# Kernel optimization log

Measured on AMD Instinct MI355X. Metric: run time of the kernel, lower is better.

## Reference

```python
import jax, jax.numpy as jnp
import numpy as np

N, E, V, H, HEADS, L, B = 20000, 320000, 100, 128, 3, 2, 200
NEG = 0.2   # leaky_relu negative_slope
EPS = 1e-5  # LayerNorm eps


def _mean_nodes(x, gid):
    # dgl.mean_nodes: per-graph mean of node features
    s = jax.ops.segment_sum(x, gid, num_segments=B)
    c = jax.ops.segment_sum(jnp.ones((x.shape[0], 1), x.dtype), gid, num_segments=B)
    return s / jnp.maximum(c, 1.0)


def _gat_layer(h, src, dst, Wn, bn, att, Ws, b, gamma, beta):
    # weight_node: Linear(H, H*HEADS)
    wv = (h @ Wn + bn).reshape(-1, HEADS, H)
    u = wv[src]  # [E, heads, H] gathered src features
    # attn = leaky_relu(sum(cat(u, v) * w_att)) split into u/v halves (no concat materialized)
    attn = (jnp.einsum('ehd,hd->eh', u, att[:, :H])
            + jnp.einsum('ehd,hd->eh', wv[dst], att[:, H:]))
    attn = jax.nn.leaky_relu(attn, NEG)  # [E, heads]
    # segment softmax over incoming edges of each dst node (mailbox softmax)
    m = jax.ops.segment_max(attn, dst, num_segments=N)
    m = jnp.where(jnp.isfinite(m), m, 0.0)
    e = jnp.exp(attn - m[dst])
    s = jax.ops.segment_sum(e, dst, num_segments=N)
    score = e / s[dst]
    agg = jax.ops.segment_sum(score[:, :, None] * u, dst, num_segments=N)  # [N, heads, H]
    res = agg.reshape(-1, HEADS * H) @ Ws + b
    # DGL leaves zero-in-degree nodes with zero reduced features (reduce_func never runs)
    has_in = jax.ops.segment_sum(jnp.ones((E,), h.dtype), dst, num_segments=N) > 0
    res = jnp.where(has_in[:, None], res, 0.0)
    x = res + h  # residual, then LayerNorm, relu (dropout is eval-mode identity)
    mu = jnp.mean(x, -1, keepdims=True)
    var = jnp.var(x, -1, keepdims=True)
    x = (x - mu) * jax.lax.rsqrt(var + EPS) * gamma + beta
    return jax.nn.relu(x)


def _gru_dir(x, Wih, Whh, bih, bhh, reverse):
    # torch nn.GRU single direction; x: [B, T, in]
    def step(hprev, xt):
        gi = xt @ Wih.T + bih
        gh = hprev @ Whh.T + bhh
        ir, iz, inn = jnp.split(gi, 3, -1)
        hr, hz, hn = jnp.split(gh, 3, -1)
        r = jax.nn.sigmoid(ir + hr)
        z = jax.nn.sigmoid(iz + hz)
        n = jnp.tanh(inn + r * hn)
        hnew = (1.0 - z) * n + z * hprev
        return hnew, hnew
    h0 = jnp.zeros((x.shape[0], Whh.shape[1]), x.dtype)
    hT, ys = jax.lax.scan(step, h0, jnp.swapaxes(x, 0, 1), reverse=reverse)
    return jnp.swapaxes(ys, 0, 1), hT


def setup_inputs() -> dict:
    key = jax.random.key(0)
    k = jax.random.split(key, 16)
    sc = 0.05
    return {
        'h': jax.random.normal(k[0], (N, H), jnp.float32),
        'wid': jax.random.randint(k[1], (N,), 0, V),
        'src': jax.random.randint(k[2], (E,), 0, N),
        'dst': jax.random.randint(k[3], (E,), 0, N),
        'graph_ids': jnp.sort(jax.random.randint(k[4], (N,), 0, B)),
        'proj_W': jax.random.normal(k[5], (V + H, H), jnp.float32) * sc,
        'proj_b': jnp.zeros((H,), jnp.float32),
        'conv_Wn': jax.random.normal(k[6], (L, H, HEADS * H), jnp.float32) * sc,
        'conv_bn': jnp.zeros((L, HEADS * H), jnp.float32),
        'conv_att': jax.random.normal(k[7], (L, HEADS, 2 * H), jnp.float32) * sc,
        'conv_Ws': jax.random.normal(k[8], (L, HEADS * H, H), jnp.float32) * sc,
        'conv_b': jnp.zeros((L, H), jnp.float32),
        'conv_gamma': jnp.ones((L, H), jnp.float32),
        'conv_beta': jnp.zeros((L, H), jnp.float32),
        'gru_Wih0': jax.random.normal(k[9], (2, 3 * H, H), jnp.float32) * sc,
        'gru_Whh0': jax.random.normal(k[10], (2, 3 * H, H), jnp.float32) * sc,
        'gru_bih0': jnp.zeros((2, 3 * H), jnp.float32),
        'gru_bhh0': jnp.zeros((2, 3 * H), jnp.float32),
        'gru_Wih1': jax.random.normal(k[11], (2, 3 * H, 2 * H), jnp.float32) * sc,
        'gru_Whh1': jax.random.normal(k[12], (2, 3 * H, H), jnp.float32) * sc,
        'gru_bih1': jnp.zeros((2, 3 * H), jnp.float32),
        'gru_bhh1': jnp.zeros((2, 3 * H), jnp.float32),
    }


def reference(h, wid, src, dst, graph_ids, proj_W, proj_b, conv_Wn, conv_bn, conv_att, conv_Ws, conv_b, conv_gamma, conv_beta, gru_Wih0, gru_Whh0, gru_bih0, gru_bhh0, gru_Wih1, gru_Whh1, gru_bih1, gru_bhh1):
    one_hot = jax.nn.one_hot(wid, V, dtype=h.dtype)
    hcur = jnp.concatenate([one_hot, h], -1) @ proj_W + proj_b  # project
    readouts = [_mean_nodes(hcur, graph_ids)]
    for l in range(L):
        hcur = _gat_layer(hcur, src, dst, conv_Wn[l], conv_bn[l], conv_att[l],
                          conv_Ws[l], conv_b[l], conv_gamma[l], conv_beta[l])
        readouts.append(_mean_nodes(hcur, graph_ids))
    x = jnp.stack(readouts, 1)  # [B, L+1, H] GRU readout sequence
    finals = []
    for (Wih, Whh, bih, bhh) in ((gru_Wih0, gru_Whh0, gru_bih0, gru_bhh0),
                                 (gru_Wih1, gru_Whh1, gru_bih1, gru_bhh1)):
        yf, hf = _gru_dir(x, Wih[0], Whh[0], bih[0], bhh[0], False)
        yb, hb = _gru_dir(x, Wih[1], Whh[1], bih[1], bhh[1], True)
        x = jnp.concatenate([yf, yb], -1)
        finals += [hf, hb]
    # torch returns h_n [num_layers*2, B, H]; module takes mean over dim 0
    return jnp.mean(jnp.stack(finals, 0), 0)  # [B, H]
```

## Files before the change

### kernel.cpp

```cpp
#include <hip/hip_runtime.h>
#include <cstddef>
#include <cstdint>

static constexpr int Nn    = 20000;
static constexpr int Ee    = 320000;
static constexpr int Vv    = 100;
static constexpr int Hh    = 128;
static constexpr int HEADS = 3;
static constexpr int Bb    = 200;
static constexpr float NEG = 0.2f;
static constexpr float EPS = 1e-5f;

typedef short bf16x8 __attribute__((ext_vector_type(8)));
typedef float f32x4  __attribute__((ext_vector_type(4)));

__device__ inline unsigned short bf16_rne(float x) {
    unsigned u = __builtin_bit_cast(unsigned, x);
    u += 0x7FFFu + ((u >> 16) & 1u);
    return (unsigned short)(u >> 16);
}
__device__ inline float bf16_f(unsigned short h) {
    unsigned u = ((unsigned)h) << 16;
    return __builtin_bit_cast(float, u);
}
__device__ inline float bf_lo(unsigned u) { return __builtin_bit_cast(float, u << 16); }
__device__ inline float bf_hi(unsigned u) { return __builtin_bit_cast(float, u & 0xFFFF0000u); }
__device__ inline float lrelu(float a) { return a >= 0.f ? a : NEG * a; }
__device__ inline float sigmoidf(float x) { return 1.f / (1.f + __expf(-x)); }

__global__ __launch_bounds__(1024) void scan_offsets(const int* __restrict__ deg,
                                                     int* __restrict__ offs,
                                                     int* __restrict__ cur) {
    __shared__ int sums[1024];
    const int tid = threadIdx.x;
    const int per = (Nn + 1023) >> 10;
    int begin = tid * per;
    int end = begin + per; if (end > Nn) end = Nn;
    if (begin > Nn) begin = Nn;
    int s = 0;
    for (int i = begin; i < end; i++) s += deg[i];
    sums[tid] = s;
    __syncthreads();
    for (int off = 1; off < 1024; off <<= 1) {
        int v = (tid >= off) ? sums[tid - off] : 0;
        __syncthreads();
        sums[tid] += v;
        __syncthreads();
    }
    int run = sums[tid] - s;
    for (int i = begin; i < end; i++) {
        offs[i] = run; cur[i] = run;
        run += deg[i];
    }
    if (end == Nn) offs[Nn] = run;
}

__global__ void fill_csr(const int* __restrict__ dst, const int* __restrict__ src,
                         int* __restrict__ cur, int* __restrict__ csrc) {
    for (int i = blockIdx.x * blockDim.x + threadIdx.x; i < Ee; i += gridDim.x * blockDim.x) {
        int p = atomicAdd(&cur[dst[i]], 1);
        csrc[p] = src[i];
    }
}

struct PrepArgs {
    const float *projW, *convWn, *convWs, *convAtt, *convBn, *convB;
    const float *Wih0, *Whh0, *Wih1, *Whh1;
    const int *gid, *dst;
    unsigned short *pBth, *pBtl;
    unsigned short *WfTh0, *WfTl0, *WfTh1, *WfTl1;
    float *vavd, *vc, *biasF;
    float *WihT0, *WhhT0, *WihT1, *WhhT1;
    int *goffs, *deg;
};

__device__ inline void wsplit(const float* B, int K, int N, int idx,
                              unsigned short* Bth, unsigned short* Btl) {
    int k = idx / N, n = idx - k * N;
    float v = B[idx];
    unsigned short h = bf16_rne(v);
    unsigned short l = bf16_rne(v - bf16_f(h));
    Bth[(size_t)n * K + k] = h;
    Btl[(size_t)n * K + k] = l;
}
__device__ inline void gruT(const float* W, int K, int idx, float* WT) {
    int d = idx / (384 * K);
    int r = idx - d * 384 * K;
    int j = r / K, k = r - j * K;
    WT[(size_t)d * K * 384 + (size_t)k * 384 + j] = W[idx];
}

__global__ void prep_all(PrepArgs a) {
    int i = blockIdx.x * blockDim.x + threadIdx.x;
    if (i < 16384) { wsplit(a.projW, 128, 128, i, a.pBth, a.pBtl); return; } i -= 16384;
#pragma unroll
    for (int l = 0; l < 2; l++) {
        if (i < 49152) {
            int k = i >> 7, c = i & 127;
            int h = k >> 7, i_ = k & 127;
            const float* wn = a.convWn + (size_t)l * 49152 + (size_t)i_ * 384 + h * 128;
            const float* ws = a.convWs + (size_t)l * 49152 + (size_t)(h * 128) * 128 + c;
            float v = 0.f;
            for (int j = 0; j < 128; j++) v += wn[j] * ws[(size_t)j * 128];
            unsigned short hi = bf16_rne(v);
            unsigned short lo = bf16_rne(v - bf16_f(hi));
            unsigned short* th = l ? a.WfTh1 : a.WfTh0;
            unsigned short* tl = l ? a.WfTl1 : a.WfTl0;
            th[(size_t)c * 384 + k] = hi;
            tl[(size_t)c * 384 + k] = lo;
            return;
        }
        i -= 49152;
    }
    if (i < 1536) {
        int l = i / 768, r = i % 768;
        int sd = r / 384, rr = r % 384, h = rr >> 7, i_ = rr & 127;
        const float* wn = a.convWn + (size_t)l * 49152 + (size_t)i_ * 384 + h * 128;
        const float* at = a.convAtt + l * 768 + h * 256 + sd * 128;
        float v = 0.f;
        for (int j = 0; j < 128; j++) v += wn[j] * at[j];
        a.vavd[i] = v;
        return;
    } i -= 1536;
    if (i < 12) {
        int l = i / 6, r = i % 6, sd = r / 3, h = r % 3;
        const float* bn = a.convBn + l * 384 + h * 128;
        const float* at = a.convAtt + l * 768 + h * 256 + sd * 128;
        float v = 0.f;
        for (int j = 0; j < 128; j++) v += bn[j] * at[j];
        a.vc[i] = v;
        return;
    } i -= 12;
    if (i < 256) {
        int l = i >> 7, c = i & 127;
        const float* bn = a.convBn + l * 384;
        const float* ws = a.convWs + (size_t)l * 49152 + c;
        float v = a.convB[l * 128 + c];
        for (int k = 0; k < 384; k++) v += bn[k] * ws[(size_t)k * 128];
        a.biasF[i] = v;
        return;
    } i -= 256;
    if (i < 98304)  { gruT(a.Wih0, 128, i, a.WihT0); return; }  i -= 98304;
    if (i < 98304)  { gruT(a.Whh0, 128, i, a.WhhT0); return; }  i -= 98304;
    if (i < 196608) { gruT(a.Wih1, 256, i, a.WihT1); return; }  i -= 196608;
    if (i < 98304)  { gruT(a.Whh1, 128, i, a.WhhT1); return; }  i -= 98304;
    if (i < Nn) {
        int g = a.gid[i];
        if (i == 0) { for (int b = 0; b <= g; b++) a.goffs[b] = 0; }
        else { int pg = a.gid[i - 1]; for (int b = pg + 1; b <= g; b++) a.goffs[b] = i; }
        if (i == Nn - 1) { for (int b = g + 1; b <= Bb; b++) a.goffs[b] = Nn; }
        return;
    } i -= Nn;
    if (i < Ee) atomicAdd(&a.deg[a.dst[i]], 1);
}

struct GArgs {
    const float* A; const unsigned short* Bth; const unsigned short* Btl;
    const float* bias; int M, K;
    const int* wid; const float* projW;
    const int* deg; const float* gamma; const float* beta;
    float* hcur;
    const int* gid; float* reado;
    const float* vavd; const float* vc;
    float* adf; float* addf;
    unsigned short* hb;
};

template <int MODE>
__global__ __launch_bounds__(256) void gemm_fused(GArgs a) {
    __shared__ unsigned short As_hi[32][40];
    __shared__ unsigned short As_lo[32][40];
    __shared__ unsigned short Bs_hi[128][40];
    __shared__ unsigned short Bs_lo[128][40];
    __shared__ float ytile[32][132];
    __shared__ float sred[6][32][4];
    __shared__ int sgid[32];
    const int tid  = threadIdx.x;
    const int row0 = blockIdx.y * 32;
    const int wn   = tid >> 6;
    const int L    = tid & 63;
    const int lrow = L & 15;
    const int lq   = L >> 4;
    const int K = a.K;

    f32x4 acc[2][2];
#pragma unroll
    for (int i = 0; i < 2; i++)
#pragma unroll
        for (int j = 0; j < 2; j++) acc[i][j] = (f32x4){0.f, 0.f, 0.f, 0.f};

    for (int kb = 0; kb < K; kb += 32) {
        {
            int m  = tid >> 3;
            int kq = (tid & 7) * 4;
            float4 v = *(const float4*)(a.A + (size_t)(row0 + m) * K + kb + kq);
            unsigned short h0 = bf16_rne(v.x), h1 = bf16_rne(v.y),
                           h2 = bf16_rne(v.z), h3 = bf16_rne(v.w);
            *(short4*)&As_hi[m][kq] = make_short4((short)h0, (short)h1, (short)h2, (short)h3);
            *(short4*)&As_lo[m][kq] = make_short4((short)bf16_rne(v.x - bf16_f(h0)),
                                                  (short)bf16_rne(v.y - bf16_f(h1)),
                                                  (short)bf16_rne(v.z - bf16_f(h2)),
                                                  (short)bf16_rne(v.w - bf16_f(h3)));
        }
        {
            int n  = tid >> 1;
            int kh = (tid & 1) * 16;
            const unsigned short* sh = a.Bth + (size_t)n * K + kb + kh;
            const unsigned short* sl = a.Btl + (size_t)n * K + kb + kh;
            *(float4*)&Bs_hi[n][kh]     = *(const float4*)sh;
            *(float4*)&Bs_hi[n][kh + 8] = *(const float4*)(sh + 8);
            *(float4*)&Bs_lo[n][kh]     = *(const float4*)sl;
            *(float4*)&Bs_lo[n][kh + 8] = *(const float4*)(sl + 8);
        }
        __syncthreads();
        bf16x8 ah[2], al[2], bh[2], bl[2];
#pragma unroll
        for (int mi = 0; mi < 2; mi++) {
            int r = mi * 16 + lrow;
            ah[mi] = *(const bf16x8*)&As_hi[r][lq * 8];
            al[mi] = *(const bf16x8*)&As_lo[r][lq * 8];
        }
#pragma unroll
        for (int ni = 0; ni < 2; ni++) {
            int r = wn * 32 + ni * 16 + lrow;
            bh[ni] = *(const bf16x8*)&Bs_hi[r][lq * 8];
            bl[ni] = *(const bf16x8*)&Bs_lo[r][lq * 8];
        }
#pragma unroll
        for (int mi = 0; mi < 2; mi++)
#pragma unroll
            for (int ni = 0; ni < 2; ni++) {
                acc[mi][ni] = __builtin_amdgcn_mfma_f32_16x16x32_bf16(ah[mi], bh[ni], acc[mi][ni], 0, 0, 0);
                acc[mi][ni] = __builtin_amdgcn_mfma_f32_16x16x32_bf16(ah[mi], bl[ni], acc[mi][ni], 0, 0, 0);
                acc[mi][ni] = __builtin_amdgcn_mfma_f32_16x16x32_bf16(al[mi], bh[ni], acc[mi][ni], 0, 0, 0);
            }
        __syncthreads();
    }

#pragma unroll
    for (int ni = 0; ni < 2; ni++) {
        float bb = a.bias[wn * 32 + ni * 16 + lrow];
#pragma unroll
        for (int mi = 0; mi < 2; mi++)
#pragma unroll
            for (int r = 0; r < 4; r++) acc[mi][ni][r] += bb;
    }

    if constexpr (MODE == 0) {
#pragma unroll
        for (int mi = 0; mi < 2; mi++)
#pragma unroll
            for (int r = 0; r < 4; r++) {
                int lr = mi * 16 + lq * 4 + r;
                int row = row0 + lr;
                int wi = a.wid[row];
#pragma unroll
                for (int ni = 0; ni < 2; ni++) {
                    int c = wn * 32 + ni * 16 + lrow;
                    float y = acc[mi][ni][r] + a.projW[(size_t)wi * 128 + c];
                    acc[mi][ni][r] = y;
                    a.hcur[(size_t)row * 128 + c] = y;
                    ytile[lr][c] = y;
                }
            }
    }

    if constexpr (MODE == 2) {
        __shared__ float red1[32][4], red2[32][4];
        float g4[2], be4[2];
#pragma unroll
        for (int ni = 0; ni < 2; ni++) {
            int c = wn * 32 + ni * 16 + lrow;
            g4[ni] = a.gamma[c]; be4[ni] = a.beta[c];
        }
#pragma unroll
        for (int mi = 0; mi < 2; mi++)
#pragma unroll
            for (int r = 0; r < 4; r++) {
                int lr = mi * 16 + lq * 4 + r;
                int row = row0 + lr;
                int dg = a.deg[row];
#pragma unroll
                for (int ni = 0; ni < 2; ni++) {
                    int c = wn * 32 + ni * 16 + lrow;
                    float hold = a.hcur[(size_t)row * 128 + c];
                    acc[mi][ni][r] = hold + (dg > 0 ? acc[mi][ni][r] : 0.f);
                }
            }
#pragma unroll
        for (int mi = 0; mi < 2; mi++)
#pragma unroll
            for (int r = 0; r < 4; r++) {
                float ps = acc[mi][0][r] + acc[mi][1][r];
#pragma unroll
                for (int o = 1; o < 16; o <<= 1) ps += __shfl_xor(ps, o, 64);
                if (lrow == 0) red1[mi * 16 + lq * 4 + r][wn] = ps;
            }
        __syncthreads();
#pragma unroll
        for (int mi = 0; mi < 2; mi++)
#pragma unroll
            for (int r = 0; r < 4; r++) {
                int lr = mi * 16 + lq * 4 + r;
                float mu = (red1[lr][0] + red1[lr][1] + red1[lr][2] + red1[lr][3]) * (1.f / 128.f);
                float qs = 0.f;
#pragma unroll
                for (int ni = 0; ni < 2; ni++) {
                    float dx = acc[mi][ni][r] - mu;
                    qs += dx * dx;
                }
#pragma unroll
                for (int o = 1; o < 16; o <<= 1) qs += __shfl_xor(qs, o, 64);
                if (lrow == 0) red2[lr][wn] = qs;
            }
        __syncthreads();
#pragma unroll
        for (int mi = 0; mi < 2; mi++)
#pragma unroll
            for (int r = 0; r < 4; r++) {
                int lr = mi * 16 + lq * 4 + r;
                int row = row0 + lr;
                float mu = (red1[lr][0] + red1[lr][1] + red1[lr][2] + red1[lr][3]) * (1.f / 128.f);
                float var = (red2[lr][0] + red2[lr][1] + red2[lr][2] + red2[lr][3]) * (1.f / 128.f);
                float rs = rsqrtf(var + EPS);
#pragma unroll
                for (int ni = 0; ni < 2; ni++) {
                    int c = wn * 32 + ni * 16 + lrow;
                    float y = fmaxf((acc[mi][ni][r] - mu) * rs * g4[ni] + be4[ni], 0.f);
                    acc[mi][ni][r] = y;
                    a.hcur[(size_t)row * 128 + c] = y;
                    ytile[lr][c] = y;
                }
            }
    }

    if (tid < 32) sgid[tid] = a.gid[row0 + tid];

    const bool dots = (a.vavd != nullptr);
    if (dots) {
        float vv0[6], vv1[6];
#pragma unroll
        for (int d = 0; d < 6; d++) {
            vv0[d] = a.vavd[d * 128 + wn * 32 + lrow];
            vv1[d] = a.vavd[d * 128 + wn * 32 + 16 + lrow];
        }
#pragma unroll
        for (int d = 0; d < 6; d++) {
#pragma unroll
            for (int mi = 0; mi < 2; mi++)
#pragma unroll
                for (int r = 0; r < 4; r++) {
                    float ps = acc[mi][0][r] * vv0[d] + acc[mi][1][r] * vv1[d];
#pragma unroll
                    for (int o = 1; o < 16; o <<= 1) ps += __shfl_xor(ps, o, 64);
                    if (lrow == 0) sred[d][mi * 16 + lq * 4 + r][wn] = ps;
                }
        }
    }
    __syncthreads();

    {
        int j = tid & 127, hh = tid >> 7;
        float sum = 0.f; int curg = -1;
        for (int r = hh * 16; r < hh * 16 + 16; r++) {
            int g = sgid[r];
            if (g != curg) {
                if (curg >= 0) atomicAdd(&a.reado[(size_t)curg * 128 + j], sum);
                sum = 0.f; curg = g;
            }
            sum += ytile[r][j];
        }
        if (curg >= 0) atomicAdd(&a.reado[(size_t)curg * 128 + j], sum);
    }

    if (dots) {
        if (tid < 192) {
            int row = tid & 31, d = tid >> 5;
            float s = sred[d][row][0] + sred[d][row][1] + sred[d][row][2] + sred[d][row][3]
                    + a.vc[d];
            int node = row0 + row;
            int sd = d / 3, h = d - sd * 3;
            float* dstp = sd ? a.addf : a.adf;
            dstp[(size_t)node * 4 + h] = s;
        }
        {
            int row = tid >> 3, c0 = (tid & 7) * 16;
            unsigned* dst = (unsigned*)(a.hb + (size_t)(row0 + row) * 128 + c0);
#pragma unroll
            for (int q = 0; q < 8; q++) {
                unsigned lo = bf16_rne(ytile[row][c0 + 2 * q]);
                unsigned hi = bf16_rne(ytile[row][c0 + 2 * q + 1]);
                dst[q] = lo | (hi << 16);
            }
        }
    }
}

__global__ __launch_bounds__(256) void gat_gather(const unsigned short* __restrict__ hb,
                                                  const float4* __restrict__ ad,
                                                  const float4* __restrict__ add,
                                                  const int* __restrict__ offs,
                                                  const int* __restrict__ csrc,
                                                  float* __restrict__ T) {
    __shared__ float4 slot[4][64];
    const int n = (blockIdx.x * 256 + threadIdx.x) >> 6;
    const int wv_ = threadIdx.x >> 6;
    const int L = threadIdx.x & 63;
    if (n >= Nn) return;
    const int start = offs[n];
    const int deg = offs[n + 1] - start;
    float2* o2 = (float2*)(T + (size_t)n * 384);
    if (deg == 0) {
        float2 z = make_float2(0.f, 0.f);
        o2[L] = z; o2[64 + L] = z; o2[128 + L] = z;
        return;
    }
    const float4 adn = add[n];
    float2 t0 = make_float2(0.f, 0.f), t1 = t0, t2 = t0;

    if (deg <= 64) {
        int sn = 0; float e0 = 0.f, e1 = 0.f, e2 = 0.f;
        if (L < deg) {
            sn = csrc[start + L];
            float4 a4 = ad[sn];
            e0 = __expf(lrelu(a4.x + adn.x));
            e1 = __expf(lrelu(a4.y + adn.y));
            e2 = __expf(lrelu(a4.z + adn.z));
        }
        float s0 = e0, s1 = e1, s2 = e2;
#pragma unroll
        for (int o = 32; o > 0; o >>= 1) {
            s0 += __shfl_xor(s0, o, 64);
            s1 += __shfl_xor(s1, o, 64);
            s2 += __shfl_xor(s2, o, 64);
        }
        slot[wv_][L] = make_float4(__builtin_bit_cast(float, sn),
                                   e0 / s0, e1 / s1, e2 / s2);
        __builtin_amdgcn_wave_barrier();
#pragma unroll 2
        for (int j = 0; j < deg; j++) {
            float4 sc = slot[wv_][j];
            int s_n = __builtin_bit_cast(int, sc.x);
            unsigned u = ((const unsigned*)(hb + (size_t)s_n * 128))[L];
            float x0 = bf_lo(u), x1 = bf_hi(u);
            t0.x += sc.y * x0; t0.y += sc.y * x1;
            t1.x += sc.z * x0; t1.y += sc.z * x1;
            t2.x += sc.w * x0; t2.y += sc.w * x1;
        }
    } else {
        float s0 = 0.f, s1 = 0.f, s2 = 0.f;
        for (int i = L; i < deg; i += 64) {
            int sn = csrc[start + i];
            float4 a4 = ad[sn];
            s0 += __expf(lrelu(a4.x + adn.x));
            s1 += __expf(lrelu(a4.y + adn.y));
            s2 += __expf(lrelu(a4.z + adn.z));
        }
#pragma unroll
        for (int o = 32; o > 0; o >>= 1) {
            s0 += __shfl_xor(s0, o, 64);
            s1 += __shfl_xor(s1, o, 64);
            s2 += __shfl_xor(s2, o, 64);
        }
        float i0 = 1.f / s0, i1 = 1.f / s1, i2 = 1.f / s2;
        for (int base = 0; base < deg; base += 64) {
            int cnt = deg - base; if (cnt > 64) cnt = 64;
            if (L < cnt) {
                int sn = csrc[start + base + L];
                float4 a4 = ad[sn];
                slot[wv_][L] = make_float4(__builtin_bit_cast(float, sn),
                                           __expf(lrelu(a4.x + adn.x)) * i0,
                                           __expf(lrelu(a4.y + adn.y)) * i1,
                                           __expf(lrelu(a4.z + adn.z)) * i2);
            }
            __builtin_amdgcn_wave_barrier();
            for (int j = 0; j < cnt; j++) {
                float4 sc = slot[wv_][j];
                int s_n = __builtin_bit_cast(int, sc.x);
                unsigned u = ((const unsigned*)(hb + (size_t)s_n * 128))[L];
                float x0 = bf_lo(u), x1 = bf_hi(u);
                t0.x += sc.y * x0; t0.y += sc.y * x1;
                t1.x += sc.z * x0; t1.y += sc.z * x1;
                t2.x += sc.w * x0; t2.y += sc.w * x1;
            }
            __builtin_amdgcn_wave_barrier();
        }
    }
    o2[L] = t0; o2[64 + L] = t1; o2[128 + L] = t2;
}

__global__ __launch_bounds__(768) void gru_all(const float* __restrict__ reado,
                                               const int* __restrict__ goffs,
                                               const float* __restrict__ WihT0,
                                               const float* __restrict__ WhhT0,
                                               const float* __restrict__ bih0,
                                               const float* __restrict__ bhh0,
                                               const float* __restrict__ WihT1,
                                               const float* __restrict__ WhhT1,
                                               const float* __restrict__ bih1,
                                               const float* __restrict__ bhh1,
                                               float* __restrict__ out) {
    const int b = blockIdx.x;
    const int tid = threadIdx.x;
    const int dir = tid / 384;
    const int j = tid - dir * 384;
    __shared__ float xs[3][128];
    __shared__ float y0s[3][256];
    __shared__ float hs[2][128];
    __shared__ float gil[2][384], ghl[2][384];
    __shared__ float fin01[2][128];
    if (tid < 128) {
        int cnt = goffs[b + 1] - goffs[b];
        float invc = 1.f / fmaxf((float)cnt, 1.f);
#pragma unroll
        for (int t = 0; t < 3; t++)
            xs[t][tid] = reado[(size_t)t * Bb * Hh + (size_t)b * Hh + tid] * invc;
    }
    if (j < 128) hs[dir][j] = 0.f;
    __syncthreads();
    {
        const float* Wi = WihT0 + (size_t)dir * 128 * 384;
        const float* Wh = WhhT0 + (size_t)dir * 128 * 384;
        float gi[3];
        gi[0] = gi[1] = gi[2] = bih0[dir * 384 + j];
        for (int k = 0; k < 128; k++) {
            float w = Wi[(size_t)k * 384 + j];
            gi[0] += w * xs[0][k]; gi[1] += w * xs[1][k]; gi[2] += w * xs[2][k];
        }
        const float bhj = bhh0[dir * 384 + j];
        for (int step = 0; step < 3; step++) {
            int t = dir ? 2 - step : step;
            float g = bhj;
            for (int k = 0; k < 128; k++) g += Wh[(size_t)k * 384 + j] * hs[dir][k];
            ghl[dir][j] = g;
            gil[dir][j] = gi[t];
            __syncthreads();
            if (j < 128) {
                float r = sigmoidf(gil[dir][j] + ghl[dir][j]);
                float z = sigmoidf(gil[dir][j + 128] + ghl[dir][j + 128]);
                float nn2 = tanhf(gil[dir][j + 256] + r * ghl[dir][j + 256]);
                float hnew = (1.f - z) * nn2 + z * hs[dir][j];
                hs[dir][j] = hnew;
                y0s[t][dir * 128 + j] = hnew;
                if (step == 2) fin01[dir][j] = hnew;
            }
            __syncthreads();
        }
    }
    if (j < 128) hs[dir][j] = 0.f;
    {
        const float* Wi = WihT1 + (size_t)dir * 256 * 384;
        const float* Wh = WhhT1 + (size_t)dir * 128 * 384;
        float gi[3];
        gi[0] = gi[1] = gi[2] = bih1[dir * 384 + j];
        for (int k = 0; k < 256; k++) {
            float w = Wi[(size_t)k * 384 + j];
            gi[0] += w * y0s[0][k]; gi[1] += w * y0s[1][k]; gi[2] += w * y0s[2][k];
        }
        const float bhj = bhh1[dir * 384 + j];
        __syncthreads();
        for (int step = 0; step < 3; step++) {
            int t = dir ? 2 - step : step;
            float g = bhj;
            for (int k = 0; k < 128; k++) g += Wh[(size_t)k * 384 + j] * hs[dir][k];
            ghl[dir][j] = g;
            gil[dir][j] = gi[t];
            __syncthreads();
            if (j < 128) {
                float r = sigmoidf(gil[dir][j] + ghl[dir][j]);
                float z = sigmoidf(gil[dir][j + 128] + ghl[dir][j + 128]);
                float nn2 = tanhf(gil[dir][j + 256] + r * ghl[dir][j + 256]);
                float hnew = (1.f - z) * nn2 + z * hs[dir][j];
                hs[dir][j] = hnew;
                if (step == 2) xs[dir][j] = hnew;
            }
            __syncthreads();
        }
    }
    if (tid < 128)
        out[(size_t)b * Hh + tid] = 0.25f * (fin01[0][tid] + fin01[1][tid] +
                                             xs[0][tid] + xs[1][tid]);
}

extern "C" void kernel_launch(void* const* d_in, const int* in_sizes, int n_in,
                              void* d_out, int out_size, void* d_ws, size_t ws_size,
                              hipStream_t stream) {
    const float* h      = (const float*)d_in[0];
    const int*   wid    = (const int*)d_in[1];
    const int*   src    = (const int*)d_in[2];
    const int*   dst    = (const int*)d_in[3];
    const int*   gid    = (const int*)d_in[4];
    const float* projW  = (const float*)d_in[5];
    const float* projB  = (const float*)d_in[6];
    const float* convWn = (const float*)d_in[7];
    const float* convBn = (const float*)d_in[8];
    const float* convAtt= (const float*)d_in[9];
    const float* convWs = (const float*)d_in[10];
    const float* convB  = (const float*)d_in[11];
    const float* convG  = (const float*)d_in[12];
    const float* convBe = (const float*)d_in[13];
    const float* Wih0   = (const float*)d_in[14];
    const float* Whh0   = (const float*)d_in[15];
    const float* bih0   = (const float*)d_in[16];
    const float* bhh0   = (const float*)d_in[17];
    const float* Wih1   = (const float*)d_in[18];
    const float* Whh1   = (const float*)d_in[19];
    const float* bih1   = (const float*)d_in[20];
    const float* bhh1   = (const float*)d_in[21];
    float* out = (float*)d_out;

    char* p = (char*)d_ws;
    auto align16 = [&]() { p = (char*)(((uintptr_t)p + 15) & ~(uintptr_t)15); };
    auto alloc_f = [&](size_t n) { align16(); float* r = (float*)p; p += n * sizeof(float); return r; };
    auto alloc_i = [&](size_t n) { align16(); int* r = (int*)p; p += n * sizeof(int); return r; };
    auto alloc_s = [&](size_t n) { align16(); unsigned short* r = (unsigned short*)p; p += n * sizeof(unsigned short); return r; };
    float* hcur  = alloc_f((size_t)Nn * 128);
    float* T     = alloc_f((size_t)Nn * 384);
    float* adbuf = alloc_f((size_t)Nn * 4);
    float* addbuf= alloc_f((size_t)Nn * 4);
    float* reado = alloc_f((size_t)3 * Bb * Hh);
    int* deg  = alloc_i(Nn);
    const size_t zero_bytes = (size_t)3 * Bb * Hh * sizeof(float) + Nn * sizeof(int);
    float* WihT0 = alloc_f((size_t)2 * 128 * 384);
    float* WhhT0 = alloc_f((size_t)2 * 128 * 384);
    float* WihT1 = alloc_f((size_t)2 * 256 * 384);
    float* WhhT1 = alloc_f((size_t)2 * 128 * 384);
    float* vavd  = alloc_f(1536);
    float* vc    = alloc_f(12);
    float* biasF = alloc_f(256);
    int* offs = alloc_i(Nn + 1);
    int* cur  = alloc_i(Nn);
    int* csrc = alloc_i(Ee);
    int* goffs = alloc_i(Bb + 1);
    unsigned short* hb = alloc_s((size_t)Nn * 128);
    unsigned short* pBth = alloc_s(128 * 128);
    unsigned short* pBtl = alloc_s(128 * 128);
    unsigned short* WfTh[2] = { alloc_s(128 * 384), alloc_s(128 * 384) };
    unsigned short* WfTl[2] = { alloc_s(128 * 384), alloc_s(128 * 384) };

    hipMemsetAsync(reado, 0, zero_bytes, stream);

    PrepArgs pa;
    pa.projW = projW + (size_t)Vv * Hh;
    pa.convWn = convWn; pa.convWs = convWs; pa.convAtt = convAtt;
    pa.convBn = convBn; pa.convB = convB;
    pa.Wih0 = Wih0; pa.Whh0 = Whh0; pa.Wih1 = Wih1; pa.Whh1 = Whh1;
    pa.gid = gid; pa.dst = dst;
    pa.pBth = pBth; pa.pBtl = pBtl;
    pa.WfTh0 = WfTh[0]; pa.WfTl0 = WfTl[0]; pa.WfTh1 = WfTh[1]; pa.WfTl1 = WfTl[1];
    pa.vavd = vavd; pa.vc = vc; pa.biasF = biasF;
    pa.WihT0 = WihT0; pa.WhhT0 = WhhT0; pa.WihT1 = WihT1; pa.WhhT1 = WhhT1;
    pa.goffs = goffs; pa.deg = deg;
    const int prep_total = 16384 + 2 * 49152 + 1536 + 12 + 256 + 98304 + 98304 + 196608 + 98304 + Nn + Ee;
    prep_all<<<(prep_total + 255) / 256, 256, 0, stream>>>(pa);

    scan_offsets<<<1, 1024, 0, stream>>>(deg, offs, cur);
    fill_csr<<<1250, 256, 0, stream>>>(dst, src, cur, csrc);

    {
        GArgs g = {};
        g.A = h; g.Bth = pBth; g.Btl = pBtl; g.bias = projB;
        g.M = Nn; g.K = 128;
        g.wid = wid; g.projW = projW; g.hcur = hcur;
        g.gid = gid; g.reado = reado;
        g.vavd = vavd; g.vc = vc; g.adf = adbuf; g.addf = addbuf; g.hb = hb;
        gemm_fused<0><<<dim3(1, Nn / 32), 256, 0, stream>>>(g);
    }

    const int nwaveblocks = (Nn * 64 + 255) / 256;
    for (int l = 0; l < 2; l++) {
        gat_gather<<<nwaveblocks, 256, 0, stream>>>(hb, (const float4*)adbuf, (const float4*)addbuf,
                                                    offs, csrc, T);
        {
            GArgs g = {};
            g.A = T; g.Bth = WfTh[l]; g.Btl = WfTl[l]; g.bias = biasF + l * 128;
            g.M = Nn; g.K = 384;
            g.deg = deg; g.gamma = convG + l * Hh; g.beta = convBe + l * Hh;
            g.hcur = hcur;
            g.gid = gid; g.reado = reado + (size_t)(l + 1) * Bb * Hh;
            if (l == 0) { g.vavd = vavd + 768; g.vc = vc + 6; g.adf = adbuf; g.addf = addbuf; g.hb = hb; }
            gemm_fused<2><<<dim3(1, Nn / 32), 256, 0, stream>>>(g);
        }
    }

    gru_all<<<Bb, 768, 0, stream>>>(reado, goffs, WihT0, WhhT0, bih0, bhh0,
                                    WihT1, WhhT1, bih1, bhh1, out);
}
```

Measured before the change: 371.8 us.

## Fuse GAT edge gather with output GEMM and LayerNorm into one per-layer kernel

Each GAT layer's gather/softmax-aggregation kernel and the following GEMM+LayerNorm kernel are merged into a single kernel. Aggregated features are split into bf16 hi/lo parts and kept in shared memory as the GEMM A operand, so the fp32 intermediate T buffer no longer has to be written to and read back from global memory. The tile shrinks to 16 rows per block, with 4 waves each gathering 4 nodes. The hb and attention-dot buffers are double-buffered so a layer never overwrites its own input. In exchange, blocks are smaller and each GEMM tile reloads the full weight matrix, which raises weight traffic and may reduce MFMA efficiency.

```diff
diff --git a/kernel.cpp b/kernel.cpp
--- a/kernel.cpp
+++ b/kernel.cpp
@@ -158,7 +158,6 @@
     const float* A; const unsigned short* Bth; const unsigned short* Btl;
     const float* bias; int M, K;
     const int* wid; const float* projW;
-    const int* deg; const float* gamma; const float* beta;
     float* hcur;
     const int* gid; float* reado;
     const float* vavd; const float* vc;
@@ -166,8 +165,7 @@
     unsigned short* hb;
 };
 
-template <int MODE>
-__global__ __launch_bounds__(256) void gemm_fused(GArgs a) {
+__global__ __launch_bounds__(256) void gemm_proj(GArgs a) {
     __shared__ unsigned short As_hi[32][40];
     __shared__ unsigned short As_lo[32][40];
     __shared__ unsigned short Bs_hi[128][40];
@@ -176,7 +174,7 @@
     __shared__ float sred[6][32][4];
     __shared__ int sgid[32];
     const int tid  = threadIdx.x;
-    const int row0 = blockIdx.y * 32;
+    const int row0 = blockIdx.x * 32;
     const int wn   = tid >> 6;
     const int L    = tid & 63;
     const int lrow = L & 15;
@@ -246,98 +244,26 @@
             for (int r = 0; r < 4; r++) acc[mi][ni][r] += bb;
     }
 
-    if constexpr (MODE == 0) {
-#pragma unroll
-        for (int mi = 0; mi < 2; mi++)
-#pragma unroll
-            for (int r = 0; r < 4; r++) {
-                int lr = mi * 16 + lq * 4 + r;
-                int row = row0 + lr;
-                int wi = a.wid[row];
-#pragma unroll
-                for (int ni = 0; ni < 2; ni++) {
-                    int c = wn * 32 + ni * 16 + lrow;
-                    float y = acc[mi][ni][r] + a.projW[(size_t)wi * 128 + c];
-                    acc[mi][ni][r] = y;
-                    a.hcur[(size_t)row * 128 + c] = y;
-                    ytile[lr][c] = y;
-                }
+#pragma unroll
+    for (int mi = 0; mi < 2; mi++)
+#pragma unroll
+        for (int r = 0; r < 4; r++) {
+            int lr = mi * 16 + lq * 4 + r;
+            int row = row0 + lr;
+            int wi = a.wid[row];
+#pragma unroll
+            for (int ni = 0; ni < 2; ni++) {
+                int c = wn * 32 + ni * 16 + lrow;
+                float y = acc[mi][ni][r] + a.projW[(size_t)wi * 128 + c];
+                acc[mi][ni][r] = y;
+                a.hcur[(size_t)row * 128 + c] = y;
+                ytile[lr][c] = y;
             }
-    }
-
-    if constexpr (MODE == 2) {
-        __shared__ float red1[32][4], red2[32][4];
-        float g4[2], be4[2];
-#pragma unroll
-        for (int ni = 0; ni < 2; ni++) {
-            int c = wn * 32 + ni * 16 + lrow;
-            g4[ni] = a.gamma[c]; be4[ni] = a.beta[c];
-        }
-#pragma unroll
-        for (int mi = 0; mi < 2; mi++)
-#pragma unroll
-            for (int r = 0; r < 4; r++) {
-                int lr = mi * 16 + lq * 4 + r;
-                int row = row0 + lr;
-                int dg = a.deg[row];
-#pragma unroll
-                for (int ni = 0; ni < 2; ni++) {
-                    int c = wn * 32 + ni * 16 + lrow;
-                    float hold = a.hcur[(size_t)row * 128 + c];
-                    acc[mi][ni][r] = hold + (dg > 0 ? acc[mi][ni][r] : 0.f);
-                }
-            }
-#pragma unroll
-        for (int mi = 0; mi < 2; mi++)
-#pragma unroll
-            for (int r = 0; r < 4; r++) {
-                float ps = acc[mi][0][r] + acc[mi][1][r];
-#pragma unroll
-                for (int o = 1; o < 16; o <<= 1) ps += __shfl_xor(ps, o, 64);
-                if (lrow == 0) red1[mi * 16 + lq * 4 + r][wn] = ps;
-            }
-        __syncthreads();
-#pragma unroll
-        for (int mi = 0; mi < 2; mi++)
-#pragma unroll
-            for (int r = 0; r < 4; r++) {
-                int lr = mi * 16 + lq * 4 + r;
-                float mu = (red1[lr][0] + red1[lr][1] + red1[lr][2] + red1[lr][3]) * (1.f / 128.f);
-                float qs = 0.f;
-#pragma unroll
-                for (int ni = 0; ni < 2; ni++) {
-                    float dx = acc[mi][ni][r] - mu;
-                    qs += dx * dx;
-                }
-#pragma unroll
-                for (int o = 1; o < 16; o <<= 1) qs += __shfl_xor(qs, o, 64);
-                if (lrow == 0) red2[lr][wn] = qs;
-            }
-        __syncthreads();
-#pragma unroll
-        for (int mi = 0; mi < 2; mi++)
-#pragma unroll
-            for (int r = 0; r < 4; r++) {
-                int lr = mi * 16 + lq * 4 + r;
-                int row = row0 + lr;
-                float mu = (red1[lr][0] + red1[lr][1] + red1[lr][2] + red1[lr][3]) * (1.f / 128.f);
-                float var = (red2[lr][0] + red2[lr][1] + red2[lr][2] + red2[lr][3]) * (1.f / 128.f);
-                float rs = rsqrtf(var + EPS);
-#pragma unroll
-                for (int ni = 0; ni < 2; ni++) {
-                    int c = wn * 32 + ni * 16 + lrow;
-                    float y = fmaxf((acc[mi][ni][r] - mu) * rs * g4[ni] + be4[ni], 0.f);
-                    acc[mi][ni][r] = y;
-                    a.hcur[(size_t)row * 128 + c] = y;
-                    ytile[lr][c] = y;
-                }
-            }
-    }
+        }
 
     if (tid < 32) sgid[tid] = a.gid[row0 + tid];
 
-    const bool dots = (a.vavd != nullptr);
-    if (dots) {
+    {
         float vv0[6], vv1[6];
 #pragma unroll
         for (int d = 0; d < 6; d++) {
@@ -373,9 +299,282 @@
         if (curg >= 0) atomicAdd(&a.reado[(size_t)curg * 128 + j], sum);
     }
 
+    if (tid < 192) {
+        int row = tid & 31, d = tid >> 5;
+        float s = sred[d][row][0] + sred[d][row][1] + sred[d][row][2] + sred[d][row][3]
+                + a.vc[d];
+        int node = row0 + row;
+        int sd = d / 3, h = d - sd * 3;
+        float* dstp = sd ? a.addf : a.adf;
+        dstp[(size_t)node * 4 + h] = s;
+    }
+    {
+        int row = tid >> 3, c0 = (tid & 7) * 16;
+        unsigned* dst = (unsigned*)(a.hb + (size_t)(row0 + row) * 128 + c0);
+#pragma unroll
+        for (int q = 0; q < 8; q++) {
+            unsigned lo = bf16_rne(ytile[row][c0 + 2 * q]);
+            unsigned hi = bf16_rne(ytile[row][c0 + 2 * q + 1]);
+            dst[q] = lo | (hi << 16);
+        }
+    }
+}
+
+struct LArgs {
+    const unsigned short* hbin;
+    const float4* ad; const float4* add;
+    const int* offs; const int* csrc;
+    const unsigned short* Bth; const unsigned short* Btl;
+    const float* biasF;
+    const float* gamma; const float* beta;
+    float* hcur;
+    const int* gid; float* reado;
+    const float* vavd; const float* vc;
+    float* adf; float* addf;
+    unsigned short* hbout;
+};
+
+__global__ __launch_bounds__(256) void gat_layer(LArgs a) {
+    __shared__ unsigned short Ah[16][392];
+    __shared__ unsigned short Al[16][392];
+    __shared__ unsigned short Bh[128][40];
+    __shared__ unsigned short Bl[128][40];
+    __shared__ float4 slot[4][64];
+    __shared__ float ytile[16][132];
+    __shared__ float sred[6][16][4];
+    __shared__ float red1[16][4], red2[16][4];
+    __shared__ int sgid[16];
+    __shared__ int sdeg[16];
+    const int tid  = threadIdx.x;
+    const int row0 = blockIdx.x * 16;
+    const int w    = tid >> 6;
+    const int L    = tid & 63;
+    const int lrow = L & 15;
+    const int lq   = L >> 4;
+
+    for (int nn = 0; nn < 4; nn++) {
+        const int lr = w * 4 + nn;
+        const int n = row0 + lr;
+        const int start = a.offs[n];
+        const int deg = a.offs[n + 1] - start;
+        if (L == 0) sdeg[lr] = deg;
+        float2 t0 = make_float2(0.f, 0.f), t1 = t0, t2 = t0;
+        if (deg > 0) {
+            const float4 adn = a.add[n];
+            if (deg <= 64) {
+                int sn = 0; float e0 = 0.f, e1 = 0.f, e2 = 0.f;
+                if (L < deg) {
+                    sn = a.csrc[start + L];
+                    float4 a4 = a.ad[sn];
+                    e0 = __expf(lrelu(a4.x + adn.x));
+                    e1 = __expf(lrelu(a4.y + adn.y));
+                    e2 = __expf(lrelu(a4.z + adn.z));
+                }
+                float s0 = e0, s1 = e1, s2 = e2;
+#pragma unroll
+                for (int o = 32; o > 0; o >>= 1) {
+                    s0 += __shfl_xor(s0, o, 64);
+                    s1 += __shfl_xor(s1, o, 64);
+                    s2 += __shfl_xor(s2, o, 64);
+                }
+                slot[w][L] = make_float4(__builtin_bit_cast(float, sn),
+                                         e0 / s0, e1 / s1, e2 / s2);
+                __builtin_amdgcn_wave_barrier();
+                for (int j = 0; j < deg; j++) {
+                    float4 sc = slot[w][j];
+                    int s_n = __builtin_bit_cast(int, sc.x);
+                    unsigned u = ((const unsigned*)a.hbin)[(size_t)s_n * 64 + L];
+                    float x0 = bf_lo(u), x1 = bf_hi(u);
+                    t0.x += sc.y * x0; t0.y += sc.y * x1;
+                    t1.x += sc.z * x0; t1.y += sc.z * x1;
+                    t2.x += sc.w * x0; t2.y += sc.w * x1;
+                }
+                __builtin_amdgcn_wave_barrier();
+            } else {
+                float s0 = 0.f, s1 = 0.f, s2 = 0.f;
+                for (int i = L; i < deg; i += 64) {
+                    int sn = a.csrc[start + i];
+                    float4 a4 = a.ad[sn];
+                    s0 += __expf(lrelu(a4.x + adn.x));
+                    s1 += __expf(lrelu(a4.y + adn.y));
+                    s2 += __expf(lrelu(a4.z + adn.z));
+                }
+#pragma unroll
+                for (int o = 32; o > 0; o >>= 1) {
+                    s0 += __shfl_xor(s0, o, 64);
+                    s1 += __shfl_xor(s1, o, 64);
+                    s2 += __shfl_xor(s2, o, 64);
+                }
+                float i0 = 1.f / s0, i1 = 1.f / s1, i2 = 1.f / s2;
+                for (int base = 0; base < deg; base += 64) {
+                    int cnt = deg - base; if (cnt > 64) cnt = 64;
+                    if (L < cnt) {
+                        int sn = a.csrc[start + base + L];
+                        float4 a4 = a.ad[sn];
+                        slot[w][L] = make_float4(__builtin_bit_cast(float, sn),
+                                                 __expf(lrelu(a4.x + adn.x)) * i0,
+                                                 __expf(lrelu(a4.y + adn.y)) * i1,
+                                                 __expf(lrelu(a4.z + adn.z)) * i2);
+                    }
+                    __builtin_amdgcn_wave_barrier();
+                    for (int j = 0; j < cnt; j++) {
+                        float4 sc = slot[w][j];
+                        int s_n = __builtin_bit_cast(int, sc.x);
+                        unsigned u = ((const unsigned*)a.hbin)[(size_t)s_n * 64 + L];
+                        float x0 = bf_lo(u), x1 = bf_hi(u);
+                        t0.x += sc.y * x0; t0.y += sc.y * x1;
+                        t1.x += sc.z * x0; t1.y += sc.z * x1;
+                        t2.x += sc.w * x0; t2.y += sc.w * x1;
+                    }
+                    __builtin_amdgcn_wave_barrier();
+                }
+            }
+        }
+        unsigned* ah32 = (unsigned*)&Ah[lr][0];
+        unsigned* al32 = (unsigned*)&Al[lr][0];
+        float2 tv[3] = {t0, t1, t2};
+#pragma unroll
+        for (int hd = 0; hd < 3; hd++) {
+            unsigned short hx = bf16_rne(tv[hd].x);
+            unsigned short hy = bf16_rne(tv[hd].y);
+            unsigned short lx = bf16_rne(tv[hd].x - bf16_f(hx));
+            unsigned short ly = bf16_rne(tv[hd].y - bf16_f(hy));
+            ah32[hd * 64 + L] = (unsigned)hx | ((unsigned)hy << 16);
+            al32[hd * 64 + L] = (unsigned)lx | ((unsigned)ly << 16);
+        }
+    }
+    if (tid < 16) sgid[tid] = a.gid[row0 + tid];
+    __syncthreads();
+
+    f32x4 acc[2];
+    acc[0] = (f32x4){0.f, 0.f, 0.f, 0.f};
+    acc[1] = (f32x4){0.f, 0.f, 0.f, 0.f};
+    for (int kb = 0; kb < 384; kb += 32) {
+        {
+            int n  = tid >> 1;
+            int kh = (tid & 1) * 16;
+            const unsigned short* sh = a.Bth + (size_t)n * 384 + kb + kh;
+            const unsigned short* sl = a.Btl + (size_t)n * 384 + kb + kh;
+            *(float4*)&Bh[n][kh]     = *(const float4*)sh;
+            *(float4*)&Bh[n][kh + 8] = *(const float4*)(sh + 8);
+            *(float4*)&Bl[n][kh]     = *(const float4*)sl;
+            *(float4*)&Bl[n][kh + 8] = *(const float4*)(sl + 8);
+        }
+        __syncthreads();
+        bf16x8 ah = *(const bf16x8*)&Ah[lrow][kb + lq * 8];
+        bf16x8 al_ = *(const bf16x8*)&Al[lrow][kb + lq * 8];
+        bf16x8 bh[2], bl[2];
+#pragma unroll
+        for (int ni = 0; ni < 2; ni++) {
+            int r = w * 32 + ni * 16 + lrow;
+            bh[ni] = *(const bf16x8*)&Bh[r][lq * 8];
+            bl[ni] = *(const bf16x8*)&Bl[r][lq * 8];
+        }
+#pragma unroll
+        for (int ni = 0; ni < 2; ni++) {
+            acc[ni] = __builtin_amdgcn_mfma_f32_16x16x32_bf16(ah, bh[ni], acc[ni], 0, 0, 0);
+            acc[ni] = __builtin_amdgcn_mfma_f32_16x16x32_bf16(ah, bl[ni], acc[ni], 0, 0, 0);
+            acc[ni] = __builtin_amdgcn_mfma_f32_16x16x32_bf16(al_, bh[ni], acc[ni], 0, 0, 0);
+        }
+        __syncthreads();
+    }
+
+    float g4[2], be4[2], bf4[2];
+#pragma unroll
+    for (int ni = 0; ni < 2; ni++) {
+        int c = w * 32 + ni * 16 + lrow;
+        g4[ni] = a.gamma[c]; be4[ni] = a.beta[c]; bf4[ni] = a.biasF[c];
+    }
+#pragma unroll
+    for (int r = 0; r < 4; r++) {
+        int lr = lq * 4 + r;
+        int row = row0 + lr;
+        int dg = sdeg[lr];
+#pragma unroll
+        for (int ni = 0; ni < 2; ni++) {
+            int c = w * 32 + ni * 16 + lrow;
+            float hold = a.hcur[(size_t)row * 128 + c];
+            acc[ni][r] = hold + (dg > 0 ? acc[ni][r] + bf4[ni] : 0.f);
+        }
+    }
+#pragma unroll
+    for (int r = 0; r < 4; r++) {
+        float ps = acc[0][r] + acc[1][r];
+#pragma unroll
+        for (int o = 1; o < 16; o <<= 1) ps += __shfl_xor(ps, o, 64);
+        if (lrow == 0) red1[lq * 4 + r][w] = ps;
+    }
+    __syncthreads();
+#pragma unroll
+    for (int r = 0; r < 4; r++) {
+        int lr = lq * 4 + r;
+        float mu = (red1[lr][0] + red1[lr][1] + red1[lr][2] + red1[lr][3]) * (1.f / 128.f);
+        float qs = 0.f;
+#pragma unroll
+        for (int ni = 0; ni < 2; ni++) {
+            float dx = acc[ni][r] - mu;
+            qs += dx * dx;
+        }
+#pragma unroll
+        for (int o = 1; o < 16; o <<= 1) qs += __shfl_xor(qs, o, 64);
+        if (lrow == 0) red2[lr][w] = qs;
+    }
+    __syncthreads();
+#pragma unroll
+    for (int r = 0; r < 4; r++) {
+        int lr = lq * 4 + r;
+        int row = row0 + lr;
+        float mu = (red1[lr][0] + red1[lr][1] + red1[lr][2] + red1[lr][3]) * (1.f / 128.f);
+        float var = (red2[lr][0] + red2[lr][1] + red2[lr][2] + red2[lr][3]) * (1.f / 128.f);
+        float rs = rsqrtf(var + EPS);
+#pragma unroll
+        for (int ni = 0; ni < 2; ni++) {
+            int c = w * 32 + ni * 16 + lrow;
+            float y = fmaxf((acc[ni][r] - mu) * rs * g4[ni] + be4[ni], 0.f);
+            acc[ni][r] = y;
+            a.hcur[(size_t)row * 128 + c] = y;
+            ytile[lr][c] = y;
+        }
+    }
+
+    const bool dots = (a.vavd != nullptr);
     if (dots) {
-        if (tid < 192) {
-            int row = tid & 31, d = tid >> 5;
+        float vv0[6], vv1[6];
+#pragma unroll
+        for (int d = 0; d < 6; d++) {
+            vv0[d] = a.vavd[d * 128 + w * 32 + lrow];
+            vv1[d] = a.vavd[d * 128 + w * 32 + 16 + lrow];
+        }
+#pragma unroll
+        for (int d = 0; d < 6; d++) {
+#pragma unroll
+            for (int r = 0; r < 4; r++) {
+                float ps = acc[0][r] * vv0[d] + acc[1][r] * vv1[d];
+#pragma unroll
+                for (int o = 1; o < 16; o <<= 1) ps += __shfl_xor(ps, o, 64);
+                if (lrow == 0) sred[d][lq * 4 + r][w] = ps;
+            }
+        }
+    }
+    __syncthreads();
+
+    {
+        int j = tid & 127, hh = tid >> 7;
+        float sum = 0.f; int curg = -1;
+        for (int r = hh * 8; r < hh * 8 + 8; r++) {
+            int g = sgid[r];
+            if (g != curg) {
+                if (curg >= 0) atomicAdd(&a.reado[(size_t)curg * 128 + j], sum);
+                sum = 0.f; curg = g;
+            }
+            sum += ytile[r][j];
+        }
+        if (curg >= 0) atomicAdd(&a.reado[(size_t)curg * 128 + j], sum);
+    }
+
+    if (dots) {
+        if (tid < 96) {
+            int row = tid & 15, d = tid >> 4;
             float s = sred[d][row][0] + sred[d][row][1] + sred[d][row][2] + sred[d][row][3]
                     + a.vc[d];
             int node = row0 + row;
@@ -383,110 +582,13 @@
             float* dstp = sd ? a.addf : a.adf;
             dstp[(size_t)node * 4 + h] = s;
         }
-        {
-            int row = tid >> 3, c0 = (tid & 7) * 16;
-            unsigned* dst = (unsigned*)(a.hb + (size_t)(row0 + row) * 128 + c0);
-#pragma unroll
-            for (int q = 0; q < 8; q++) {
-                unsigned lo = bf16_rne(ytile[row][c0 + 2 * q]);
-                unsigned hi = bf16_rne(ytile[row][c0 + 2 * q + 1]);
-                dst[q] = lo | (hi << 16);
-            }
-        }
-    }
-}
-
-__global__ __launch_bounds__(256) void gat_gather(const unsigned short* __restrict__ hb,
-                                                  const float4* __restrict__ ad,
-                                                  const float4* __restrict__ add,
-                                                  const int* __restrict__ offs,
-                                                  const int* __restrict__ csrc,
-                                                  float* __restrict__ T) {
-    __shared__ float4 slot[4][64];
-    const int n = (blockIdx.x * 256 + threadIdx.x) >> 6;
-    const int wv_ = threadIdx.x >> 6;
-    const int L = threadIdx.x & 63;
-    if (n >= Nn) return;
-    const int start = offs[n];
-    const int deg = offs[n + 1] - start;
-    float2* o2 = (float2*)(T + (size_t)n * 384);
-    if (deg == 0) {
-        float2 z = make_float2(0.f, 0.f);
-        o2[L] = z; o2[64 + L] = z; o2[128 + L] = z;
-        return;
-    }
-    const float4 adn = add[n];
-    float2 t0 = make_float2(0.f, 0.f), t1 = t0, t2 = t0;
-
-    if (deg <= 64) {
-        int sn = 0; float e0 = 0.f, e1 = 0.f, e2 = 0.f;
-        if (L < deg) {
-            sn = csrc[start + L];
-            float4 a4 = ad[sn];
-            e0 = __expf(lrelu(a4.x + adn.x));
-            e1 = __expf(lrelu(a4.y + adn.y));
-            e2 = __expf(lrelu(a4.z + adn.z));
-        }
-        float s0 = e0, s1 = e1, s2 = e2;
-#pragma unroll
-        for (int o = 32; o > 0; o >>= 1) {
-            s0 += __shfl_xor(s0, o, 64);
-            s1 += __shfl_xor(s1, o, 64);
-            s2 += __shfl_xor(s2, o, 64);
-        }
-        slot[wv_][L] = make_float4(__builtin_bit_cast(float, sn),
-                                   e0 / s0, e1 / s1, e2 / s2);
-        __builtin_amdgcn_wave_barrier();
-#pragma unroll 2
-        for (int j = 0; j < deg; j++) {
-            float4 sc = slot[wv_][j];
-            int s_n = __builtin_bit_cast(int, sc.x);
-            unsigned u = ((const unsigned*)(hb + (size_t)s_n * 128))[L];
-            float x0 = bf_lo(u), x1 = bf_hi(u);
-            t0.x += sc.y * x0; t0.y += sc.y * x1;
-            t1.x += sc.z * x0; t1.y += sc.z * x1;
-            t2.x += sc.w * x0; t2.y += sc.w * x1;
-        }
-    } else {
-        float s0 = 0.f, s1 = 0.f, s2 = 0.f;
-        for (int i = L; i < deg; i += 64) {
-            int sn = csrc[start + i];
-            float4 a4 = ad[sn];
-            s0 += __expf(lrelu(a4.x + adn.x));
-            s1 += __expf(lrelu(a4.y + adn.y));
-            s2 += __expf(lrelu(a4.z + adn.z));
-        }
-#pragma unroll
-        for (int o = 32; o > 0; o >>= 1) {
-            s0 += __shfl_xor(s0, o, 64);
-            s1 += __shfl_xor(s1, o, 64);
-            s2 += __shfl_xor(s2, o, 64);
-        }
-        float i0 = 1.f / s0, i1 = 1.f / s1, i2 = 1.f / s2;
-        for (int base = 0; base < deg; base += 64) {
-            int cnt = deg - base; if (cnt > 64) cnt = 64;
-            if (L < cnt) {
-                int sn = csrc[start + base + L];
-                float4 a4 = ad[sn];
-                slot[wv_][L] = make_float4(__builtin_bit_cast(float, sn),
-                                           __expf(lrelu(a4.x + adn.x)) * i0,
-                                           __expf(lrelu(a4.y + adn.y)) * i1,
-                                           __expf(lrelu(a4.z + adn.z)) * i2);
-            }
-            __builtin_amdgcn_wave_barrier();
-            for (int j = 0; j < cnt; j++) {
-                float4 sc = slot[wv_][j];
-                int s_n = __builtin_bit_cast(int, sc.x);
-                unsigned u = ((const unsigned*)(hb + (size_t)s_n * 128))[L];
-                float x0 = bf_lo(u), x1 = bf_hi(u);
-                t0.x += sc.y * x0; t0.y += sc.y * x1;
-                t1.x += sc.z * x0; t1.y += sc.z * x1;
-                t2.x += sc.w * x0; t2.y += sc.w * x1;
-            }
-            __builtin_amdgcn_wave_barrier();
-        }
-    }
-    o2[L] = t0; o2[64 + L] = t1; o2[128 + L] = t2;
+        for (int idx = tid; idx < 16 * 64; idx += 256) {
+            int row = idx >> 6, c = idx & 63;
+            unsigned lo = bf16_rne(ytile[row][2 * c]);
+            unsigned hi = bf16_rne(ytile[row][2 * c + 1]);
+            ((unsigned*)a.hbout)[(size_t)(row0 + row) * 64 + c] = lo | (hi << 16);
+        }
+    }
 }
 
 __global__ __launch_bounds__(768) void gru_all(const float* __restrict__ reado,
@@ -615,9 +717,10 @@
     auto alloc_i = [&](size_t n) { align16(); int* r = (int*)p; p += n * sizeof(int); return r; };
     auto alloc_s = [&](size_t n) { align16(); unsigned short* r = (unsigned short*)p; p += n * sizeof(unsigned short); return r; };
     float* hcur  = alloc_f((size_t)Nn * 128);
-    float* T     = alloc_f((size_t)Nn * 384);
-    float* adbuf = alloc_f((size_t)Nn * 4);
-    float* addbuf= alloc_f((size_t)Nn * 4);
+    float* adbuf0 = alloc_f((size_t)Nn * 4);
+    float* addbuf0= alloc_f((size_t)Nn * 4);
+    float* adbuf1 = alloc_f((size_t)Nn * 4);
+    float* addbuf1= alloc_f((size_t)Nn * 4);
     float* reado = alloc_f((size_t)3 * Bb * Hh);
     int* deg  = alloc_i(Nn);
     const size_t zero_bytes = (size_t)3 * Bb * Hh * sizeof(float) + Nn * sizeof(int);
@@ -632,7 +735,8 @@
     int* cur  = alloc_i(Nn);
     int* csrc = alloc_i(Ee);
     int* goffs = alloc_i(Bb + 1);
-    unsigned short* hb = alloc_s((size_t)Nn * 128);
+    unsigned short* hb0 = alloc_s((size_t)Nn * 128);
+    unsigned short* hb1 = alloc_s((size_t)Nn * 128);
     unsigned short* pBth = alloc_s(128 * 128);
     unsigned short* pBtl = alloc_s(128 * 128);
     unsigned short* WfTh[2] = { alloc_s(128 * 384), alloc_s(128 * 384) };
@@ -663,24 +767,25 @@
         g.M = Nn; g.K = 128;
         g.wid = wid; g.projW = projW; g.hcur = hcur;
         g.gid = gid; g.reado = reado;
-        g.vavd = vavd; g.vc = vc; g.adf = adbuf; g.addf = addbuf; g.hb = hb;
-        gemm_fused<0><<<dim3(1, Nn / 32), 256, 0, stream>>>(g);
-    }
-
-    const int nwaveblocks = (Nn * 64 + 255) / 256;
+        g.vavd = vavd; g.vc = vc; g.adf = adbuf0; g.addf = addbuf0; g.hb = hb0;
+        gemm_proj<<<Nn / 32, 256, 0, stream>>>(g);
+    }
+
     for (int l = 0; l < 2; l++) {
-        gat_gather<<<nwaveblocks, 256, 0, stream>>>(hb, (const float4*)adbuf, (const float4*)addbuf,
-                                                    offs, csrc, T);
-        {
-            GArgs g = {};
-            g.A = T; g.Bth = WfTh[l]; g.Btl = WfTl[l]; g.bias = biasF + l * 128;
-            g.M = Nn; g.K = 384;
-            g.deg = deg; g.gamma = convG + l * Hh; g.beta = convBe + l * Hh;
-            g.hcur = hcur;
-            g.gid = gid; g.reado = reado + (size_t)(l + 1) * Bb * Hh;
-            if (l == 0) { g.vavd = vavd + 768; g.vc = vc + 6; g.adf = adbuf; g.addf = addbuf; g.hb = hb; }
-            gemm_fused<2><<<dim3(1, Nn / 32), 256, 0, stream>>>(g);
-        }
+        LArgs g = {};
+        g.hbin = l ? hb1 : hb0;
+        g.ad = (const float4*)(l ? adbuf1 : adbuf0);
+        g.add = (const float4*)(l ? addbuf1 : addbuf0);
+        g.offs = offs; g.csrc = csrc;
+        g.Bth = WfTh[l]; g.Btl = WfTl[l]; g.biasF = biasF + l * 128;
+        g.gamma = convG + l * Hh; g.beta = convBe + l * Hh;
+        g.hcur = hcur; g.gid = gid;
+        g.reado = reado + (size_t)(l + 1) * Bb * Hh;
+        if (l == 0) {
+            g.vavd = vavd + 768; g.vc = vc + 6;
+            g.adf = adbuf1; g.addf = addbuf1; g.hbout = hb1;
+        }
+        gat_layer<<<Nn / 16, 256, 0, stream>>>(g);
     }
 
     gru_all<<<Bb, 768, 0, stream>>>(reado, goffs, WihT0, WhhT0, bih0, bhh0,
```

After: 412.1 us. 1.11x slower.
